# Optimization experiments

Measured on AMD Instinct MI355X. Metric: run time of the kernel, lower is better.

Reference implementation:

```python
import jax, jax.numpy as jnp
import numpy as np

N = 50000          # nodes
E = 1_600_000      # edges (avg degree 32)
H = 2              # attention heads per layer
F = 64             # per-head feature dim
NC = 16            # num_classes
NEG_SLOPE = 0.2    # PyG GATConv default leaky relu slope


def setup_inputs():
    key = jax.random.key(0)
    ks = jax.random.split(key, 20)
    s = 0.05
    z = jnp.zeros
    inp = {
        'x': jax.random.normal(ks[0], (N, 64), dtype=jnp.float32),
        'edge_index': jax.random.randint(ks[1], (2, E), 0, N, dtype=jnp.int32),
        # GAT layer 1: in=64 (heads=1 concat from input), out=H*F
        'W1': jax.random.normal(ks[2], (64, H * F)) * s,
        'a_src1': jax.random.normal(ks[3], (H, F)) * s,
        'a_dst1': jax.random.normal(ks[4], (H, F)) * s,
        'b1': z((H * F,)),
        # GAT layer 2: in=H*F=128, out=H*F
        'W2': jax.random.normal(ks[5], (H * F, H * F)) * s,
        'a_src2': jax.random.normal(ks[6], (H, F)) * s,
        'a_dst2': jax.random.normal(ks[7], (H, F)) * s,
        'b2': z((H * F,)),
        # MLP head: 128 -> 512 -> 256 -> NC
        'lw1': jax.random.normal(ks[8], (H * F, 512)) * s, 'lb1': z((512,)),
        'lw2': jax.random.normal(ks[9], (512, 256)) * s, 'lb2': z((256,)),
        'lw3': jax.random.normal(ks[10], (256, NC)) * s, 'lb3': z((NC,)),
    }
    return inp


def gat_conv(x, src, dst, W, a_src, a_dst, b):
    """PyG-style GATConv (shared weights for src/dst), head concat output."""
    h = (x @ W).reshape(-1, H, F)                       # [N, H, F]
    alpha_s = jnp.einsum('nhf,hf->nh', h, a_src)        # [N, H]
    alpha_d = jnp.einsum('nhf,hf->nh', h, a_dst)
    e = jax.nn.leaky_relu(alpha_s[src] + alpha_d[dst], NEG_SLOPE)  # [E', H]
    # segment softmax over incoming edges of each dst node
    e_max = jax.ops.segment_max(e, dst, num_segments=N)            # [N, H]
    e_exp = jnp.exp(e - e_max[dst])
    denom = jax.ops.segment_sum(e_exp, dst, num_segments=N)
    alpha = e_exp / (denom[dst] + 1e-16)                            # [E', H]
    msg = h[src] * alpha[:, :, None]                                # [E', H, F]
    out = jax.ops.segment_sum(msg, dst, num_segments=N)             # [N, H, F]
    return out.reshape(N, H * F) + b


def reference(x, edge_index, W1, a_src1, a_dst1, b1, W2, a_src2, a_dst2, b2,
              lw1, lb1, lw2, lb2, lw3, lb3):
    # add self loops (PyG GATConv default)
    loop = jnp.arange(N, dtype=edge_index.dtype)
    src = jnp.concatenate([edge_index[0], loop])
    dst = jnp.concatenate([edge_index[1], loop])

    h = jax.nn.relu(gat_conv(x, src, dst, W1, a_src1, a_dst1, b1))
    emb = jax.nn.relu(gat_conv(h, src, dst, W2, a_src2, a_dst2, b2))

    z = jax.nn.relu(emb @ lw1 + lb1)
    z = jax.nn.relu(z @ lw2 + lb2)
    logits = z @ lw3 + lb3
    return emb, logits
```

## Files before the change

kernel.cpp:

```cpp
#include <hip/hip_runtime.h>

typedef __bf16 bf16f __attribute__((ext_vector_type(8)));
typedef float  f32x4 __attribute__((ext_vector_type(4)));

__device__ __forceinline__ float bf2f(unsigned short u) {
  union { unsigned int u; float f; } v;
  v.u = ((unsigned int)u) << 16;
  return v.f;
}
__device__ __forceinline__ unsigned short f2bf(float f) {
  union { float f; unsigned int u; } v; v.f = f;
  unsigned int r = v.u + 0x7FFFu + ((v.u >> 16) & 1u);
  return (unsigned short)(r >> 16);
}
__device__ __forceinline__ float bflo(unsigned int w) {
  union { unsigned int u; float f; } v; v.u = w << 16; return v.f;
}
__device__ __forceinline__ float bfhi(unsigned int w) {
  union { unsigned int u; float f; } v; v.u = w & 0xFFFF0000u; return v.f;
}

__global__ void GNNModel_general_12077448036407_kernel(int* cnt, int ncnt) {
  int i = blockIdx.x * blockDim.x + threadIdx.x;
  if (i < ncnt) cnt[i] = 0;
}

__global__ void rank_kernel(const int* __restrict__ dst, int* __restrict__ cnt,
                            unsigned short* __restrict__ rank, int E) {
  int e = blockIdx.x * blockDim.x + threadIdx.x;
  if (e < E) {
    int r = atomicAdd(&cnt[dst[e]], 1);
    rank[e] = (unsigned short)r;
  }
}

__global__ void scan1_kernel(const int* __restrict__ cnt, int* __restrict__ offs,
                             int* __restrict__ bsum, int M) {
  __shared__ int sh[256];
  int t = threadIdx.x;
  int i = blockIdx.x * 256 + t;
  int v = (i < M) ? cnt[i] : 0;
  sh[t] = v;
  __syncthreads();
  for (int off = 1; off < 256; off <<= 1) {
    int u = (t >= off) ? sh[t - off] : 0;
    __syncthreads();
    sh[t] += u;
    __syncthreads();
  }
  if (i <= M) offs[i] = sh[t] - v;
  if (t == 255) bsum[blockIdx.x] = sh[255];
}

__global__ void scan2_kernel(int* __restrict__ bsum, int NB) {
  __shared__ int sh[256];
  int t = threadIdx.x;
  int v = (t < NB) ? bsum[t] : 0;
  sh[t] = v;
  __syncthreads();
  for (int off = 1; off < 256; off <<= 1) {
    int u = (t >= off) ? sh[t - off] : 0;
    __syncthreads();
    sh[t] += u;
    __syncthreads();
  }
  if (t < NB) bsum[t] = sh[t] - v;
}

__global__ void scan3_kernel(int* __restrict__ offs, const int* __restrict__ bsum, int M) {
  int i = blockIdx.x * 256 + threadIdx.x;
  if (i <= M) offs[i] += bsum[i >> 8];
}

__global__ void place_kernel(const int* __restrict__ src, const int* __restrict__ dst,
                             const unsigned short* __restrict__ rank,
                             const int* __restrict__ offs, int* __restrict__ csr_src, int E) {
  int e = blockIdx.x * blockDim.x + threadIdx.x;
  if (e < E) {
    int p = offs[dst[e]] + (int)rank[e];
    __builtin_nontemporal_store(src[e], &csr_src[p]);
  }
}

__global__ void wpack_kernel(const float* __restrict__ W, unsigned short* __restrict__ Bw,
                             int K, int Nt) {
  int i = blockIdx.x * blockDim.x + threadIdx.x;
  if (i >= K * Nt) return;
  int n = i / K, k = i - n * K;
  Bw[i] = f2bf(W[(size_t)k * Nt + n]);
}

__launch_bounds__(256)
__global__ void m128_kernel(const void* __restrict__ A,
                            const unsigned short* __restrict__ Bw,
                            const float* __restrict__ bias, void* __restrict__ C,
                            int M, int K, int Nt, int aBF, int cBF, int relu) {
  __shared__ unsigned short As[128 * 32];
  __shared__ unsigned short Bs[128 * 32];
  int tid = threadIdx.x;
  int wid = tid >> 6, lane = tid & 63;
  int lm = lane & 15, quad = lane >> 4;
  int wr = wid >> 1, wc = wid & 1;
  int n0 = blockIdx.x * 128, m0 = blockIdx.y * 128;

  f32x4 acc[4][4];
#pragma unroll
  for (int mi = 0; mi < 4; mi++)
#pragma unroll
    for (int ni = 0; ni < 4; ni++)
#pragma unroll
      for (int i = 0; i < 4; i++) acc[mi][ni][i] = 0.0f;

  int c0 = (wid << 6) + lane;
  int c1 = c0 + 256;
  int srow = tid >> 1;
  int skc  = (tid & 1) << 4;

  for (int k0 = 0; k0 < K; k0 += 32) {
    {
      const unsigned short* g0 = Bw + (size_t)(n0 + (c0 >> 2)) * K + k0 + ((c0 & 3) << 3);
      __builtin_amdgcn_global_load_lds((const __attribute__((address_space(1))) void*)g0,
                                       (__attribute__((address_space(3))) void*)(Bs + (wid << 9)),
                                       16, 0, 0);
      const unsigned short* g1 = Bw + (size_t)(n0 + (c1 >> 2)) * K + k0 + ((c1 & 3) << 3);
      __builtin_amdgcn_global_load_lds((const __attribute__((address_space(1))) void*)g1,
                                       (__attribute__((address_space(3))) void*)(Bs + 2048 + (wid << 9)),
                                       16, 0, 0);
    }
    if (aBF) {
      int r0 = m0 + (c0 >> 2); if (r0 > M - 1) r0 = M - 1;
      const unsigned short* g0 = (const unsigned short*)A + (size_t)r0 * K + k0 + ((c0 & 3) << 3);
      __builtin_amdgcn_global_load_lds((const __attribute__((address_space(1))) void*)g0,
                                       (__attribute__((address_space(3))) void*)(As + (wid << 9)),
                                       16, 0, 0);
      int r1 = m0 + (c1 >> 2); if (r1 > M - 1) r1 = M - 1;
      const unsigned short* g1 = (const unsigned short*)A + (size_t)r1 * K + k0 + ((c1 & 3) << 3);
      __builtin_amdgcn_global_load_lds((const __attribute__((address_space(1))) void*)g1,
                                       (__attribute__((address_space(3))) void*)(As + 2048 + (wid << 9)),
                                       16, 0, 0);
    } else {
      int gm = m0 + srow;
      uint4 p0, p1;
      if (gm < M) {
        const float* Af = (const float*)A + (size_t)gm * K + k0 + skc;
        float4 r0 = *(const float4*)Af;
        float4 r1 = *(const float4*)(Af + 4);
        float4 r2 = *(const float4*)(Af + 8);
        float4 r3 = *(const float4*)(Af + 12);
        p0.x = (unsigned int)f2bf(r0.x) | ((unsigned int)f2bf(r0.y) << 16);
        p0.y = (unsigned int)f2bf(r0.z) | ((unsigned int)f2bf(r0.w) << 16);
        p0.z = (unsigned int)f2bf(r1.x) | ((unsigned int)f2bf(r1.y) << 16);
        p0.w = (unsigned int)f2bf(r1.z) | ((unsigned int)f2bf(r1.w) << 16);
        p1.x = (unsigned int)f2bf(r2.x) | ((unsigned int)f2bf(r2.y) << 16);
        p1.y = (unsigned int)f2bf(r2.z) | ((unsigned int)f2bf(r2.w) << 16);
        p1.z = (unsigned int)f2bf(r3.x) | ((unsigned int)f2bf(r3.y) << 16);
        p1.w = (unsigned int)f2bf(r3.z) | ((unsigned int)f2bf(r3.w) << 16);
      } else {
        p0.x = p0.y = p0.z = p0.w = 0u;
        p1.x = p1.y = p1.z = p1.w = 0u;
      }
      *(uint4*)&As[srow * 32 + skc] = p0;
      *(uint4*)&As[srow * 32 + skc + 8] = p1;
    }
    __syncthreads();

    bf16f afr[4], bfr[4];
#pragma unroll
    for (int mi = 0; mi < 4; mi++)
      afr[mi] = *(const bf16f*)&As[(wr * 64 + mi * 16 + lm) * 32 + quad * 8];
#pragma unroll
    for (int ni = 0; ni < 4; ni++)
      bfr[ni] = *(const bf16f*)&Bs[(wc * 64 + ni * 16 + lm) * 32 + quad * 8];
#pragma unroll
    for (int mi = 0; mi < 4; mi++)
#pragma unroll
      for (int ni = 0; ni < 4; ni++)
        acc[mi][ni] = __builtin_amdgcn_mfma_f32_16x16x32_bf16(afr[mi], bfr[ni], acc[mi][ni], 0, 0, 0);
    __syncthreads();
  }

#pragma unroll
  for (int ni = 0; ni < 4; ni++) {
    int col = n0 + wc * 64 + ni * 16 + lm;
    float bv = (bias != 0) ? bias[col] : 0.0f;
#pragma unroll
    for (int mi = 0; mi < 4; mi++) {
#pragma unroll
      for (int i = 0; i < 4; i++) {
        int row = m0 + wr * 64 + mi * 16 + quad * 4 + i;
        if (row < M) {
          float v = acc[mi][ni][i] + bv;
          if (relu) v = fmaxf(v, 0.0f);
          if (cBF) ((unsigned short*)C)[(size_t)row * Nt + col] = f2bf(v);
          else     ((float*)C)[(size_t)row * Nt + col] = v;
        }
      }
    }
  }
}

__launch_bounds__(256)
__global__ void lgemm_kernel(const unsigned short* __restrict__ A,
                             const float* __restrict__ W,
                             const float* __restrict__ bias, float* __restrict__ C,
                             int M, int K) {
  __shared__ unsigned short Bt[16 * 264];
  int tid = threadIdx.x;
  int wave = tid >> 6, lane = tid & 63;
  int lm = lane & 15, quad = lane >> 4;
  int m0 = blockIdx.x * 64;

  for (int f0 = tid * 4; f0 < K * 16; f0 += 1024) {
    float4 w4 = *(const float4*)(W + f0);
    int k = f0 >> 4, n = f0 & 15;
    Bt[(n + 0) * 264 + k] = f2bf(w4.x);
    Bt[(n + 1) * 264 + k] = f2bf(w4.y);
    Bt[(n + 2) * 264 + k] = f2bf(w4.z);
    Bt[(n + 3) * 264 + k] = f2bf(w4.w);
  }
  __syncthreads();

  f32x4 acc;
#pragma unroll
  for (int i = 0; i < 4; i++) acc[i] = 0.0f;

  int m = m0 + wave * 16 + lm;
  const unsigned short* Ap = A + (size_t)m * K;

  for (int k0 = 0; k0 < K; k0 += 32) {
    bf16f af;
#pragma unroll
    for (int j = 0; j < 8; j++) af[j] = (__bf16)0.0f;
    if (m < M) af = *(const bf16f*)(Ap + k0 + quad * 8);
    bf16f bfv = *(const bf16f*)&Bt[lm * 264 + k0 + quad * 8];
    acc = __builtin_amdgcn_mfma_f32_16x16x32_bf16(af, bfv, acc, 0, 0, 0);
  }

  float bv = bias[lm];
#pragma unroll
  for (int i = 0; i < 4; i++) {
    int row = m0 + wave * 16 + quad * 4 + i;
    if (row < M) C[(size_t)row * 16 + lm] = acc[i] + bv;
  }
}

__launch_bounds__(256)
__global__ void tgemm_kernel(const void* __restrict__ A, const float* __restrict__ W,
                             const float* __restrict__ bias, void* __restrict__ C,
                             int M, int K, int Nt, int aBF, int cBF, int relu) {
  __shared__ float As[16][132];
  __shared__ float Bs[16][136];
  int t = threadIdx.x;
  int tx = t & 15, ty = t >> 4;
  int m0 = blockIdx.x * 128, n0 = blockIdx.y * 128;

  float acc[8][8];
#pragma unroll
  for (int i = 0; i < 8; i++)
#pragma unroll
    for (int j = 0; j < 8; j++) acc[i][j] = 0.0f;

  int arow = t >> 1;
  int akc  = (t & 1) * 8;
  int bkk  = t >> 4;
  int bnn  = (t & 15) * 8;
  int gm = m0 + arow;

  for (int k0 = 0; k0 < K; k0 += 16) {
    float av[8];
    if (gm < M) {
      if (aBF) {
        const unsigned short* Ab = (const unsigned short*)A + (size_t)gm * K + k0 + akc;
        uint4 raw = *(const uint4*)Ab;
        av[0] = bflo(raw.x); av[1] = bfhi(raw.x);
        av[2] = bflo(raw.y); av[3] = bfhi(raw.y);
        av[4] = bflo(raw.z); av[5] = bfhi(raw.z);
        av[6] = bflo(raw.w); av[7] = bfhi(raw.w);
      } else {
        const float* Af = (const float*)A + (size_t)gm * K + k0 + akc;
        float4 r0 = *(const float4*)Af;
        float4 r1 = *(const float4*)(Af + 4);
        av[0] = r0.x; av[1] = r0.y; av[2] = r0.z; av[3] = r0.w;
        av[4] = r1.x; av[5] = r1.y; av[6] = r1.z; av[7] = r1.w;
      }
    } else {
#pragma unroll
      for (int j = 0; j < 8; j++) av[j] = 0.0f;
    }
#pragma unroll
    for (int j = 0; j < 8; j++) As[akc + j][arow] = av[j];

    const float* bp = W + (size_t)(k0 + bkk) * Nt + n0 + bnn;
    float4 b0 = *(const float4*)bp;
    float4 b1 = *(const float4*)(bp + 4);
    *(float4*)&Bs[bkk][bnn]     = b0;
    *(float4*)&Bs[bkk][bnn + 4] = b1;

    __syncthreads();

#pragma unroll 4
    for (int kk = 0; kk < 16; kk++) {
      float a[8], b[8];
      *(float4*)&a[0] = *(const float4*)&As[kk][ty * 8];
      *(float4*)&a[4] = *(const float4*)&As[kk][ty * 8 + 4];
      *(float4*)&b[0] = *(const float4*)&Bs[kk][tx * 8];
      *(float4*)&b[4] = *(const float4*)&Bs[kk][tx * 8 + 4];
#pragma unroll
      for (int i = 0; i < 8; i++)
#pragma unroll
        for (int j = 0; j < 8; j++)
          acc[i][j] = fmaf(a[i], b[j], acc[i][j]);
    }
    __syncthreads();
  }

  float bv[8];
#pragma unroll
  for (int j = 0; j < 8; j++) bv[j] = (bias != 0) ? bias[n0 + tx * 8 + j] : 0.0f;

#pragma unroll
  for (int i = 0; i < 8; i++) {
    int m = m0 + ty * 8 + i;
    if (m >= M) continue;
    float v[8];
#pragma unroll
    for (int j = 0; j < 8; j++) {
      float s = acc[i][j] + bv[j];
      v[j] = relu ? fmaxf(s, 0.0f) : s;
    }
    if (cBF) {
      unsigned short* Cp = (unsigned short*)C + (size_t)m * Nt + n0 + tx * 8;
      uint4 pk;
      pk.x = (unsigned int)f2bf(v[0]) | ((unsigned int)f2bf(v[1]) << 16);
      pk.y = (unsigned int)f2bf(v[2]) | ((unsigned int)f2bf(v[3]) << 16);
      pk.z = (unsigned int)f2bf(v[4]) | ((unsigned int)f2bf(v[5]) << 16);
      pk.w = (unsigned int)f2bf(v[6]) | ((unsigned int)f2bf(v[7]) << 16);
      *(uint4*)Cp = pk;
    } else {
      float* Cp = (float*)C + (size_t)m * Nt + n0 + tx * 8;
      float4 o0; o0.x = v[0]; o0.y = v[1]; o0.z = v[2]; o0.w = v[3];
      float4 o1; o1.x = v[4]; o1.y = v[5]; o1.z = v[6]; o1.w = v[7];
      *(float4*)Cp = o0;
      *(float4*)(Cp + 4) = o1;
    }
  }
}

__global__ void alphas_kernel(const unsigned short* __restrict__ hb,
                              const float* __restrict__ a_src,
                              const float* __restrict__ a_dst,
                              float2* __restrict__ aSp, float2* __restrict__ aDp, int M) {
  int gw = (blockIdx.x * blockDim.x + threadIdx.x) >> 6;
  int lane = threadIdx.x & 63;
  if (gw >= M) return;
  float h0 = bf2f(hb[(size_t)gw * 128 + lane]);
  float h1 = bf2f(hb[(size_t)gw * 128 + 64 + lane]);
  float as0 = h0 * a_src[lane];
  float as1 = h1 * a_src[64 + lane];
  float ad0 = h0 * a_dst[lane];
  float ad1 = h1 * a_dst[64 + lane];
  for (int o = 32; o; o >>= 1) {
    as0 += __shfl_xor(as0, o);
    as1 += __shfl_xor(as1, o);
    ad0 += __shfl_xor(ad0, o);
    ad1 += __shfl_xor(ad1, o);
  }
  if (lane == 0) {
    aSp[gw] = make_float2(as0, as1);
    aDp[gw] = make_float2(ad0, ad1);
  }
}

__global__ void aggregate_kernel(const unsigned short* __restrict__ hb,
                                 const float2* __restrict__ aSp,
                                 const float2* __restrict__ aDp,
                                 const int* __restrict__ csr_src, const int* __restrict__ offs,
                                 const float* __restrict__ bias,
                                 float* __restrict__ out, int M) {
  int n = (blockIdx.x * blockDim.x + threadIdx.x) >> 6;
  int lane = threadIdx.x & 63;
  if (n >= M) return;
  int g = lane >> 4;
  int q = lane & 15;
  int h0sel = (q < 8);

  float2 adn = aDp[n];
  float2 asn = aSp[n];
  float e0 = asn.x + adn.x; e0 = (e0 > 0.0f) ? e0 : 0.2f * e0;
  float e1 = asn.y + adn.y; e1 = (e1 > 0.0f) ? e1 : 0.2f * e1;
  float ws0 = expf(e0), ws1 = expf(e1);
  float wself = h0sel ? ws0 : ws1;

  float acc[8];
  if (g == 0) {
    uint4 rv = *(const uint4*)(hb + (size_t)n * 128 + q * 8);
    acc[0] = wself * bflo(rv.x); acc[1] = wself * bfhi(rv.x);
    acc[2] = wself * bflo(rv.y); acc[3] = wself * bfhi(rv.y);
    acc[4] = wself * bflo(rv.z); acc[5] = wself * bfhi(rv.z);
    acc[6] = wself * bflo(rv.w); acc[7] = wself * bfhi(rv.w);
  } else {
#pragma unroll
    for (int i = 0; i < 8; i++) acc[i] = 0.0f;
  }

  float lp0 = 0.0f, lp1 = 0.0f;
  int rs = offs[n], re = offs[n + 1];
  for (int base = rs; base < re; base += 64) {
    int cnt = re - base; if (cnt > 64) cnt = 64;
    int s = 0; float w0 = 0.0f, w1 = 0.0f;
    if (lane < cnt) {
      s = csr_src[base + lane];
      float2 a = aSp[s];
      float f0 = a.x + adn.x; f0 = (f0 > 0.0f) ? f0 : 0.2f * f0;
      float f1 = a.y + adn.y; f1 = (f1 > 0.0f) ? f1 : 0.2f * f1;
      w0 = expf(f0); w1 = expf(f1);
      lp0 += w0; lp1 += w1;
    }
    int jmax = (cnt + 3) >> 2;
#pragma unroll 2
    for (int j = 0; j < jmax; j++) {
      int el = 4 * j + g;
      int sj  = __shfl(s, el);
      float w0j = __shfl(w0, el);
      float w1j = __shfl(w1, el);
      float wj = h0sel ? w0j : w1j;
      uint4 rv = *(const uint4*)(hb + (size_t)sj * 128 + q * 8);
      acc[0] = fmaf(wj, bflo(rv.x), acc[0]);
      acc[1] = fmaf(wj, bfhi(rv.x), acc[1]);
      acc[2] = fmaf(wj, bflo(rv.y), acc[2]);
      acc[3] = fmaf(wj, bfhi(rv.y), acc[3]);
      acc[4] = fmaf(wj, bflo(rv.z), acc[4]);
      acc[5] = fmaf(wj, bfhi(rv.z), acc[5]);
      acc[6] = fmaf(wj, bflo(rv.w), acc[6]);
      acc[7] = fmaf(wj, bfhi(rv.w), acc[7]);
    }
  }
#pragma unroll
  for (int i = 0; i < 8; i++) {
    acc[i] += __shfl_xor(acc[i], 16);
    acc[i] += __shfl_xor(acc[i], 32);
  }
  for (int o = 32; o; o >>= 1) {
    lp0 += __shfl_xor(lp0, o);
    lp1 += __shfl_xor(lp1, o);
  }
  if (g == 0) {
    float linv = 1.0f / ((h0sel ? lp0 + ws0 : lp1 + ws1) + 1e-16f);
    const float* bp = bias + q * 8;
    float4 o0, o1;
    o0.x = fmaxf(acc[0] * linv + bp[0], 0.0f);
    o0.y = fmaxf(acc[1] * linv + bp[1], 0.0f);
    o0.z = fmaxf(acc[2] * linv + bp[2], 0.0f);
    o0.w = fmaxf(acc[3] * linv + bp[3], 0.0f);
    o1.x = fmaxf(acc[4] * linv + bp[4], 0.0f);
    o1.y = fmaxf(acc[5] * linv + bp[5], 0.0f);
    o1.z = fmaxf(acc[6] * linv + bp[6], 0.0f);
    o1.w = fmaxf(acc[7] * linv + bp[7], 0.0f);
    float* op = out + (size_t)n * 128 + q * 8;
    *(float4*)op = o0;
    *(float4*)(op + 4) = o1;
  }
}

extern "C" void kernel_launch(void* const* d_in, const int* in_sizes, int n_in,
                              void* d_out, int out_size, void* d_ws, size_t ws_size,
                              hipStream_t stream) {
  const int N = in_sizes[0] / 64;
  const int E = in_sizes[1] / 2;
  const float* x   = (const float*)d_in[0];
  const int*   ei  = (const int*)d_in[1];
  const float* W1  = (const float*)d_in[2];
  const float* as1 = (const float*)d_in[3];
  const float* ad1 = (const float*)d_in[4];
  const float* b1  = (const float*)d_in[5];
  const float* W2  = (const float*)d_in[6];
  const float* as2 = (const float*)d_in[7];
  const float* ad2 = (const float*)d_in[8];
  const float* b2  = (const float*)d_in[9];
  const float* lw1 = (const float*)d_in[10];
  const float* lb1 = (const float*)d_in[11];
  const float* lw2 = (const float*)d_in[12];
  const float* lb2 = (const float*)d_in[13];
  const float* lw3 = (const float*)d_in[14];
  const float* lb3 = (const float*)d_in[15];

  float* emb    = (float*)d_out;
  float* logits = (float*)d_out + (size_t)N * 128;

  char* base = (char*)d_ws;
  size_t o = 0;
  unsigned short* Wb1 = (unsigned short*)(base + o); o += ((size_t)512 * 128 * 2 + 255) & ~(size_t)255;
  unsigned short* Wb2 = (unsigned short*)(base + o); o += ((size_t)256 * 512 * 2 + 255) & ~(size_t)255;
  char* tb = base + o;

  size_t t = 0;
  unsigned short* hb = (unsigned short*)(tb + t); t += ((size_t)N * 128 * 2 + 255) & ~(size_t)255;
  float* x2f = (float*)(tb + t); t += ((size_t)N * 128 * 4 + 255) & ~(size_t)255;
  float2* aSp = (float2*)(tb + t); t += ((size_t)N * 8 + 255) & ~(size_t)255;
  float2* aDp = (float2*)(tb + t); t += ((size_t)N * 8 + 255) & ~(size_t)255;
  int* cnt  = (int*)(tb + t); t += ((size_t)N * 4 + 255) & ~(size_t)255;
  int* offs = (int*)(tb + t); t += ((size_t)(N + 1) * 4 + 255) & ~(size_t)255;
  int* bsum = (int*)(tb + t); t += ((size_t)256 * 4 + 255) & ~(size_t)255;
  unsigned short* rank = (unsigned short*)(tb + t); t += ((size_t)E * 2 + 255) & ~(size_t)255;
  int* csr  = (int*)(tb + t); t += ((size_t)E * 4 + 255) & ~(size_t)255;
  unsigned short* z1b = (unsigned short*)tb;
  unsigned short* z2b = (unsigned short*)(tb + (((size_t)N * 512 * 2 + 255) & ~(size_t)255));

  const int* esrc = ei;
  const int* edst = ei + E;

  wpack_kernel<<<(128 * 512 + 255) / 256, 256, 0, stream>>>(lw1, Wb1, 128, 512);
  wpack_kernel<<<(512 * 256 + 255) / 256, 256, 0, stream>>>(lw2, Wb2, 512, 256);

  GNNModel_general_12077448036407_kernel<<<(N + 255) / 256, 256, 0, stream>>>(cnt, N);
  int eb = (E + 255) / 256;
  rank_kernel<<<eb, 256, 0, stream>>>(edst, cnt, rank, E);
  int sb = (N + 256) / 256;
  scan1_kernel<<<sb, 256, 0, stream>>>(cnt, offs, bsum, N);
  scan2_kernel<<<1, 256, 0, stream>>>(bsum, sb);
  scan3_kernel<<<sb, 256, 0, stream>>>(offs, bsum, N);
  place_kernel<<<eb, 256, 0, stream>>>(esrc, edst, rank, offs, csr, E);

  int nb4 = (N + 3) / 4;
  int mtb = (N + 127) / 128;

  tgemm_kernel<<<dim3(mtb, 1), 256, 0, stream>>>(x, W1, (const float*)0, hb,
                                                 N, 64, 128, 0, 1, 0);
  alphas_kernel<<<nb4, 256, 0, stream>>>(hb, as1, ad1, aSp, aDp, N);
  aggregate_kernel<<<nb4, 256, 0, stream>>>(hb, aSp, aDp, csr, offs, b1, x2f, N);

  tgemm_kernel<<<dim3(mtb, 1), 256, 0, stream>>>(x2f, W2, (const float*)0, hb,
                                                 N, 128, 128, 0, 1, 0);
  alphas_kernel<<<nb4, 256, 0, stream>>>(hb, as2, ad2, aSp, aDp, N);
  aggregate_kernel<<<nb4, 256, 0, stream>>>(hb, aSp, aDp, csr, offs, b2, emb, N);

  m128_kernel<<<dim3(4, mtb), 256, 0, stream>>>(emb, Wb1, lb1, z1b,
                                                N, 128, 512, 0, 1, 1);
  m128_kernel<<<dim3(2, mtb), 256, 0, stream>>>(z1b, Wb2, lb2, z2b,
                                                N, 512, 256, 1, 1, 1);
  int mtb64 = (N + 63) / 64;
  lgemm_kernel<<<mtb64, 256, 0, stream>>>(z2b, lw3, lb3, logits, N, 256);
}
```

Before: 528.3 us.

## Fuse layer-1 GEMM with edge ranking and alphas with CSR placement

Merges independent stages into single launches by block-index partitioning: the first-layer feature GEMM shares a grid with the atomic edge-rank pass, and the first-layer attention-logit computation shares a grid with the CSR placement scatter. The two weight-pack launches also become one kernel. The aim is to cut launch count and let compute-bound and atomic/scatter-bound work run concurrently on the GPU. The cost is a dedicated fp32 GEMM path for layer 1 in place of the previous tgemm, plus mixed block types whose scheduling order is not controlled.

```diff
diff --git a/kernel.cpp b/kernel.cpp
--- a/kernel.cpp
+++ b/kernel.cpp
@@ -25,12 +25,103 @@
   if (i < ncnt) cnt[i] = 0;
 }
 
-__global__ void rank_kernel(const int* __restrict__ dst, int* __restrict__ cnt,
-                            unsigned short* __restrict__ rank, int E) {
-  int e = blockIdx.x * blockDim.x + threadIdx.x;
-  if (e < E) {
-    int r = atomicAdd(&cnt[dst[e]], 1);
-    rank[e] = (unsigned short)r;
+__global__ void wpack2_kernel(const float* __restrict__ lw1, unsigned short* __restrict__ Wb1,
+                              const float* __restrict__ lw2, unsigned short* __restrict__ Wb2) {
+  int i = blockIdx.x * blockDim.x + threadIdx.x;
+  if (i < 512 * 128) {
+    int n = i >> 7, k = i & 127;
+    Wb1[i] = f2bf(lw1[(size_t)k * 512 + n]);
+  }
+  if (i < 256 * 512) {
+    int n = i >> 9, k = i & 511;
+    Wb2[i] = f2bf(lw2[(size_t)k * 256 + n]);
+  }
+}
+
+__launch_bounds__(256)
+__global__ void gr_fused_kernel(const float* __restrict__ x, const float* __restrict__ W1,
+                                unsigned short* __restrict__ hb, int M, int gblocks,
+                                const int* __restrict__ dst, int* __restrict__ cnt,
+                                unsigned short* __restrict__ rank, int E) {
+  __shared__ float As[16][132];
+  __shared__ float Bs[16][136];
+  int bid = blockIdx.x;
+  int t = threadIdx.x;
+
+  if (bid >= gblocks) {
+    int e = (bid - gblocks) * 256 + t;
+    if (e < E) {
+      int r = atomicAdd(&cnt[dst[e]], 1);
+      rank[e] = (unsigned short)r;
+    }
+    return;
+  }
+
+  int tx = t & 15, ty = t >> 4;
+  int m0 = bid * 128;
+
+  float acc[8][8];
+#pragma unroll
+  for (int i = 0; i < 8; i++)
+#pragma unroll
+    for (int j = 0; j < 8; j++) acc[i][j] = 0.0f;
+
+  int arow = t >> 1;
+  int akc  = (t & 1) * 8;
+  int bkk  = t >> 4;
+  int bnn  = (t & 15) * 8;
+  int gm = m0 + arow;
+
+  for (int k0 = 0; k0 < 64; k0 += 16) {
+    float av[8];
+    if (gm < M) {
+      const float* Af = x + (size_t)gm * 64 + k0 + akc;
+      float4 r0 = *(const float4*)Af;
+      float4 r1 = *(const float4*)(Af + 4);
+      av[0] = r0.x; av[1] = r0.y; av[2] = r0.z; av[3] = r0.w;
+      av[4] = r1.x; av[5] = r1.y; av[6] = r1.z; av[7] = r1.w;
+    } else {
+#pragma unroll
+      for (int j = 0; j < 8; j++) av[j] = 0.0f;
+    }
+#pragma unroll
+    for (int j = 0; j < 8; j++) As[akc + j][arow] = av[j];
+
+    const float* bp = W1 + (size_t)(k0 + bkk) * 128 + bnn;
+    float4 b0 = *(const float4*)bp;
+    float4 b1 = *(const float4*)(bp + 4);
+    *(float4*)&Bs[bkk][bnn]     = b0;
+    *(float4*)&Bs[bkk][bnn + 4] = b1;
+
+    __syncthreads();
+
+#pragma unroll 4
+    for (int kk = 0; kk < 16; kk++) {
+      float a[8], b[8];
+      *(float4*)&a[0] = *(const float4*)&As[kk][ty * 8];
+      *(float4*)&a[4] = *(const float4*)&As[kk][ty * 8 + 4];
+      *(float4*)&b[0] = *(const float4*)&Bs[kk][tx * 8];
+      *(float4*)&b[4] = *(const float4*)&Bs[kk][tx * 8 + 4];
+#pragma unroll
+      for (int i = 0; i < 8; i++)
+#pragma unroll
+        for (int j = 0; j < 8; j++)
+          acc[i][j] = fmaf(a[i], b[j], acc[i][j]);
+    }
+    __syncthreads();
+  }
+
+#pragma unroll
+  for (int i = 0; i < 8; i++) {
+    int m = m0 + ty * 8 + i;
+    if (m >= M) continue;
+    unsigned short* Cp = hb + (size_t)m * 128 + tx * 8;
+    uint4 pk;
+    pk.x = (unsigned int)f2bf(acc[i][0]) | ((unsigned int)f2bf(acc[i][1]) << 16);
+    pk.y = (unsigned int)f2bf(acc[i][2]) | ((unsigned int)f2bf(acc[i][3]) << 16);
+    pk.z = (unsigned int)f2bf(acc[i][4]) | ((unsigned int)f2bf(acc[i][5]) << 16);
+    pk.w = (unsigned int)f2bf(acc[i][6]) | ((unsigned int)f2bf(acc[i][7]) << 16);
+    *(uint4*)Cp = pk;
   }
 }
 
@@ -72,22 +163,45 @@
   if (i <= M) offs[i] += bsum[i >> 8];
 }
 
-__global__ void place_kernel(const int* __restrict__ src, const int* __restrict__ dst,
-                             const unsigned short* __restrict__ rank,
-                             const int* __restrict__ offs, int* __restrict__ csr_src, int E) {
-  int e = blockIdx.x * blockDim.x + threadIdx.x;
-  if (e < E) {
-    int p = offs[dst[e]] + (int)rank[e];
-    __builtin_nontemporal_store(src[e], &csr_src[p]);
-  }
-}
-
-__global__ void wpack_kernel(const float* __restrict__ W, unsigned short* __restrict__ Bw,
-                             int K, int Nt) {
-  int i = blockIdx.x * blockDim.x + threadIdx.x;
-  if (i >= K * Nt) return;
-  int n = i / K, k = i - n * K;
-  Bw[i] = f2bf(W[(size_t)k * Nt + n]);
+__global__ void pa_fused_kernel(const unsigned short* __restrict__ hb,
+                                const float* __restrict__ a_src,
+                                const float* __restrict__ a_dst,
+                                float2* __restrict__ aSp, float2* __restrict__ aDp,
+                                int M, int ablocks,
+                                const int* __restrict__ src, const int* __restrict__ dstp,
+                                const unsigned short* __restrict__ rank,
+                                const int* __restrict__ offs, int* __restrict__ csr, int E) {
+  int bid = blockIdx.x;
+  int t = threadIdx.x;
+
+  if (bid >= ablocks) {
+    int e = (bid - ablocks) * 256 + t;
+    if (e < E) {
+      int p = offs[dstp[e]] + (int)rank[e];
+      __builtin_nontemporal_store(src[e], &csr[p]);
+    }
+    return;
+  }
+
+  int gw = (bid * 256 + t) >> 6;
+  int lane = t & 63;
+  if (gw >= M) return;
+  float h0 = bf2f(hb[(size_t)gw * 128 + lane]);
+  float h1 = bf2f(hb[(size_t)gw * 128 + 64 + lane]);
+  float as0 = h0 * a_src[lane];
+  float as1 = h1 * a_src[64 + lane];
+  float ad0 = h0 * a_dst[lane];
+  float ad1 = h1 * a_dst[64 + lane];
+  for (int o = 32; o; o >>= 1) {
+    as0 += __shfl_xor(as0, o);
+    as1 += __shfl_xor(as1, o);
+    ad0 += __shfl_xor(ad0, o);
+    ad1 += __shfl_xor(ad1, o);
+  }
+  if (lane == 0) {
+    aSp[gw] = make_float2(as0, as1);
+    aDp[gw] = make_float2(ad0, ad1);
+  }
 }
 
 __launch_bounds__(256)
@@ -509,24 +623,23 @@
   const int* esrc = ei;
   const int* edst = ei + E;
 
-  wpack_kernel<<<(128 * 512 + 255) / 256, 256, 0, stream>>>(lw1, Wb1, 128, 512);
-  wpack_kernel<<<(512 * 256 + 255) / 256, 256, 0, stream>>>(lw2, Wb2, 512, 256);
+  int eb = (E + 255) / 256;
+  int sb = (N + 256) / 256;
+  int nb4 = (N + 3) / 4;
+  int mtb = (N + 127) / 128;
 
   GNNModel_general_12077448036407_kernel<<<(N + 255) / 256, 256, 0, stream>>>(cnt, N);
-  int eb = (E + 255) / 256;
-  rank_kernel<<<eb, 256, 0, stream>>>(edst, cnt, rank, E);
-  int sb = (N + 256) / 256;
+  wpack2_kernel<<<512, 256, 0, stream>>>(lw1, Wb1, lw2, Wb2);
+
+  gr_fused_kernel<<<mtb + eb, 256, 0, stream>>>(x, W1, hb, N, mtb, edst, cnt, rank, E);
+
   scan1_kernel<<<sb, 256, 0, stream>>>(cnt, offs, bsum, N);
   scan2_kernel<<<1, 256, 0, stream>>>(bsum, sb);
   scan3_kernel<<<sb, 256, 0, stream>>>(offs, bsum, N);
-  place_kernel<<<eb, 256, 0, stream>>>(esrc, edst, rank, offs, csr, E);
-
-  int nb4 = (N + 3) / 4;
-  int mtb = (N + 127) / 128;
-
-  tgemm_kernel<<<dim3(mtb, 1), 256, 0, stream>>>(x, W1, (const float*)0, hb,
-                                                 N, 64, 128, 0, 1, 0);
-  alphas_kernel<<<nb4, 256, 0, stream>>>(hb, as1, ad1, aSp, aDp, N);
+
+  pa_fused_kernel<<<nb4 + eb, 256, 0, stream>>>(hb, as1, ad1, aSp, aDp, N, nb4,
+                                                esrc, edst, rank, offs, csr, E);
+
   aggregate_kernel<<<nb4, 256, 0, stream>>>(hb, aSp, aDp, csr, offs, b1, x2f, N);
 
   tgemm_kernel<<<dim3(mtb, 1), 256, 0, stream>>>(x2f, W2, (const float*)0, hb,
```

Measured after the change: 503.5 us. 4.7% less time.
